# Optimization experiments

Hardware: AMD Instinct MI355X
Metric: run time of the kernel (lower is better)

Reference implementation:

```python
import jax, jax.numpy as jnp
import numpy as np

N_REVIEWS = 500000
N_ITEMS = 100000
N_USERS = 200000
D = 128           # per-entity embedding dim
INPUT_DIM = 3 * D # 384
OUTPUT_DIM = 128


def setup_inputs() -> dict:
    key = jax.random.key(0)
    k1, k2, k3, k4, k5, k6 = jax.random.split(key, 6)
    review_embedding = jax.random.normal(k1, (N_REVIEWS, D), dtype=jnp.float32)
    item_embedding = jax.random.normal(k2, (N_ITEMS, D), dtype=jnp.float32)
    user_embedding = jax.random.normal(k3, (N_USERS, D), dtype=jnp.float32)
    adj_user_idx = jax.random.randint(k4, (N_REVIEWS,), 0, N_USERS, dtype=jnp.int32)
    adj_item_idx = jax.random.randint(k5, (N_REVIEWS,), 0, N_ITEMS, dtype=jnp.int32)
    agg_weights = jax.random.normal(k6, (INPUT_DIM, OUTPUT_DIM), dtype=jnp.float32) * 0.05
    return {
        "review_embedding": review_embedding,
        "item_embedding": item_embedding,
        "user_embedding": user_embedding,
        "adj_user_idx": adj_user_idx,
        "adj_item_idx": adj_item_idx,
        "agg_weights": agg_weights,
    }


def reference(review_embedding, item_embedding, user_embedding,
              adj_user_idx, adj_item_idx, agg_weights):
    # Gather neighbor embeddings (tf.nn.embedding_lookup)
    review_item = item_embedding[adj_item_idx]  # [N_reviews, D]
    review_user = user_embedding[adj_user_idx]  # [N_reviews, D]
    # Concat along feature axis -> [N_reviews, 3D], then dense + activation
    agg_vector = jnp.concatenate([review_embedding, review_user, review_item], axis=1)
    return jax.nn.relu(agg_vector @ agg_weights)
```

## Files before the change

### kernel.cpp

```cpp
#include <hip/hip_runtime.h>
#include <hip/hip_bf16.h>

#define NREV 500000
#define DIM  128
#define KDIM 384

typedef __attribute__((ext_vector_type(4))) float f32x4;
typedef __attribute__((ext_vector_type(8))) short bf16x8;

__device__ __forceinline__ unsigned short f2bf_s(float x) {
    unsigned int u = __builtin_bit_cast(unsigned int, x);
    u = (u + 0x7FFFu + ((u >> 16) & 1u)) >> 16;
    return (unsigned short)u;
}

__global__ void wconv_kernel(const float* __restrict__ W,
                             unsigned short* __restrict__ Bw) {
    int e = blockIdx.x * 256 + threadIdx.x;
    if (e < 12 * 8 * 64 * 8) {
        int j  = e & 7;
        int l  = (e >> 3) & 63;
        int fg = (e >> 9) & 7;
        int ks = e >> 12;
        int n = fg * 16 + (l & 15);
        int k = ks * 32 + ((l >> 4) << 3) + j;
        Bw[e] = f2bf_s(W[k * DIM + n]);
    }
}

__device__ __forceinline__ void gload_lds16(const void* g, void* l) {
    __builtin_amdgcn_global_load_lds(
        (const __attribute__((address_space(1))) void*)g,
        (__attribute__((address_space(3))) void*)l, 16, 0, 0);
}

__device__ __forceinline__ unsigned int pktrunc(float lo, float hi) {
    unsigned int a = __builtin_bit_cast(unsigned int, lo);
    unsigned int b = __builtin_bit_cast(unsigned int, hi);
    return (b & 0xFFFF0000u) | (a >> 16);
}
__device__ __forceinline__ bf16x8 cvt8(f32x4 a, f32x4 b) {
    union { bf16x8 v; unsigned int u[4]; } U;
    U.u[0] = pktrunc(a[0], a[1]);
    U.u[1] = pktrunc(a[2], a[3]);
    U.u[2] = pktrunc(b[0], b[1]);
    U.u[3] = pktrunc(b[2], b[3]);
    return U.v;
}

__global__ __launch_bounds__(256, 2) void agg_kernel(
    const float* __restrict__ rev,
    const float* __restrict__ item,
    const float* __restrict__ user,
    const int*   __restrict__ uidx,
    const int*   __restrict__ iidx,
    const unsigned short* __restrict__ Bw,
    float* __restrict__ out)
{
    __shared__ __align__(16) float          Atile[3][128 * 32];
    __shared__ __align__(16) unsigned short Btile[3][4096];

    const int r0   = blockIdx.x * 128;
    const int t    = threadIdx.x;
    const int wid  = t >> 6, lane = t & 63;
    const int wr   = wid >> 1, wc = wid & 1;
    const int lm   = lane & 15, lk = lane >> 4;

    const int srow = t >> 3;
    const int cswz = ((t & 7) ^ ((t >> 3) & 7)) << 2;

    const float* pr[4]; const float* pu[4]; const float* pi[4];
    #pragma unroll
    for (int it = 0; it < 4; ++it) {
        int gr = r0 + it * 32 + srow;
        if (gr >= NREV) gr = NREV - 1;
        pr[it] = rev  + (size_t)gr * DIM + cswz;
        pu[it] = user + (size_t)uidx[gr] * DIM + cswz;
        pi[it] = item + (size_t)iidx[gr] * DIM + cswz;
    }

    f32x4 acc[4][4];
    #pragma unroll
    for (int i = 0; i < 4; ++i)
        #pragma unroll
        for (int j = 0; j < 4; ++j)
            acc[i][j] = (f32x4){0.f, 0.f, 0.f, 0.f};

    const int axor  = (lm & 7) << 4;
    const int koff0 = (lk * 32) ^ axor;

    auto prefetch = [&](int s, int buf) {
        const int cb = (s & 3) * 32;
        #pragma unroll
        for (int it = 0; it < 4; ++it) {
            const float* src = ((s < 4) ? pr[it] : (s < 8) ? pu[it] : pi[it]) + cb;
            gload_lds16(src, (char*)&Atile[buf][0] + it * 4096 + t * 16);
        }
        #pragma unroll
        for (int it = 0; it < 2; ++it) {
            gload_lds16((const char*)Bw + s * 8192 + it * 4096 + t * 16,
                        (char*)&Btile[buf][0] + it * 4096 + t * 16);
        }
    };

    auto step = [&](int s) {
        const char*           la = (const char*)&Atile[s % 3][0];
        const unsigned short* lb = &Btile[s % 3][0];
        bf16x8 bfrag[4];
        #pragma unroll
        for (int nf = 0; nf < 4; ++nf)
            bfrag[nf] = *reinterpret_cast<const bf16x8*>(
                lb + (((wc * 4 + nf) * 64 + lane) << 3));
        #pragma unroll
        for (int mf = 0; mf < 4; ++mf) {
            int rb = (wr * 64 + mf * 16 + lm) * 128;
            f32x4 f0 = *reinterpret_cast<const f32x4*>(la + rb + koff0);
            f32x4 f1 = *reinterpret_cast<const f32x4*>(la + rb + (koff0 ^ 16));
            bf16x8 af = cvt8(f0, f1);
            #pragma unroll
            for (int nf = 0; nf < 4; ++nf)
                acc[mf][nf] = __builtin_amdgcn_mfma_f32_16x16x32_bf16(
                    af, bfrag[nf], acc[mf][nf], 0, 0, 0);
        }
    };

    prefetch(0, 0);
    prefetch(1, 1);

    #pragma unroll
    for (int s = 0; s < 12; ++s) {
        if (s == 11) { asm volatile("s_waitcnt vmcnt(0)" ::: "memory"); }
        else         { asm volatile("s_waitcnt vmcnt(6)" ::: "memory"); }
        __builtin_amdgcn_s_barrier();
        asm volatile("" ::: "memory");
        if (s < 10) prefetch(s + 2, (s + 2) % 3);
        step(s);
    }

    #pragma unroll
    for (int mf = 0; mf < 4; ++mf) {
        #pragma unroll
        for (int j = 0; j < 4; ++j) {
            int row = r0 + wr * 64 + mf * 16 + lk * 4 + j;
            if (row < NREV) {
                float* orow = out + (size_t)row * DIM + wc * 64;
                #pragma unroll
                for (int nf = 0; nf < 4; ++nf)
                    orow[nf * 16 + lm] = fmaxf(acc[mf][nf][j], 0.0f);
            }
        }
    }
}

extern "C" void kernel_launch(void* const* d_in, const int* in_sizes, int n_in,
                              void* d_out, int out_size, void* d_ws, size_t ws_size,
                              hipStream_t stream) {
    const float* rev  = (const float*)d_in[0];
    const float* item = (const float*)d_in[1];
    const float* user = (const float*)d_in[2];
    const int*   uidx = (const int*)d_in[3];
    const int*   iidx = (const int*)d_in[4];
    const float* W    = (const float*)d_in[5];
    unsigned short* Bw = (unsigned short*)d_ws;
    float* out = (float*)d_out;

    wconv_kernel<<<192, 256, 0, stream>>>(W, Bw);

    int nblocks = (NREV + 127) / 128;
    agg_kernel<<<nblocks, 256, 0, stream>>>(rev, item, user, uidx, iidx, Bw, out);
}
```

Before: 179.1 us.

## Load A and B fragments directly from global memory, dropping the LDS pipeline

Removes the triple-buffered LDS staging with global_load_lds and barriers. Each lane now loads its own A fragment rows and B fragments straight from global memory into registers, relying on the fully unrolled loop for latency hiding. s_setprio is added around the MFMA block, and the fp32-to-bf16 truncation now uses a single perm instruction per pair. This saves LDS traffic and block-wide synchronisation, but each wave reloads the gathered rows and weights that were previously shared, and coalescing becomes worse since each lane fetches 32-byte chunks.

```diff
diff --git a/kernel.cpp b/kernel.cpp
--- a/kernel.cpp
+++ b/kernel.cpp
@@ -28,23 +28,17 @@
     }
 }
 
-__device__ __forceinline__ void gload_lds16(const void* g, void* l) {
-    __builtin_amdgcn_global_load_lds(
-        (const __attribute__((address_space(1))) void*)g,
-        (__attribute__((address_space(3))) void*)l, 16, 0, 0);
-}
-
-__device__ __forceinline__ unsigned int pktrunc(float lo, float hi) {
-    unsigned int a = __builtin_bit_cast(unsigned int, lo);
-    unsigned int b = __builtin_bit_cast(unsigned int, hi);
-    return (b & 0xFFFF0000u) | (a >> 16);
+__device__ __forceinline__ unsigned int pk2(float lo, float hi) {
+    return __builtin_amdgcn_perm(__builtin_bit_cast(unsigned int, hi),
+                                 __builtin_bit_cast(unsigned int, lo),
+                                 0x07060302u);
 }
 __device__ __forceinline__ bf16x8 cvt8(f32x4 a, f32x4 b) {
     union { bf16x8 v; unsigned int u[4]; } U;
-    U.u[0] = pktrunc(a[0], a[1]);
-    U.u[1] = pktrunc(a[2], a[3]);
-    U.u[2] = pktrunc(b[0], b[1]);
-    U.u[3] = pktrunc(b[2], b[3]);
+    U.u[0] = pk2(a[0], a[1]);
+    U.u[1] = pk2(a[2], a[3]);
+    U.u[2] = pk2(b[0], b[1]);
+    U.u[3] = pk2(b[2], b[3]);
     return U.v;
 }
 
@@ -57,26 +51,20 @@
     const unsigned short* __restrict__ Bw,
     float* __restrict__ out)
 {
-    __shared__ __align__(16) float          Atile[3][128 * 32];
-    __shared__ __align__(16) unsigned short Btile[3][4096];
-
-    const int r0   = blockIdx.x * 128;
     const int t    = threadIdx.x;
     const int wid  = t >> 6, lane = t & 63;
     const int wr   = wid >> 1, wc = wid & 1;
     const int lm   = lane & 15, lk = lane >> 4;
+    const int r0   = blockIdx.x * 128;
 
-    const int srow = t >> 3;
-    const int cswz = ((t & 7) ^ ((t >> 3) & 7)) << 2;
-
-    const float* pr[4]; const float* pu[4]; const float* pi[4];
+    const float* baseA[3][4];
     #pragma unroll
-    for (int it = 0; it < 4; ++it) {
-        int gr = r0 + it * 32 + srow;
-        if (gr >= NREV) gr = NREV - 1;
-        pr[it] = rev  + (size_t)gr * DIM + cswz;
-        pu[it] = user + (size_t)uidx[gr] * DIM + cswz;
-        pi[it] = item + (size_t)iidx[gr] * DIM + cswz;
+    for (int mf = 0; mf < 4; ++mf) {
+        int r = r0 + wr * 64 + mf * 16 + lm;
+        if (r >= NREV) r = NREV - 1;
+        baseA[0][mf] = rev  + (size_t)r * DIM + lk * 8;
+        baseA[1][mf] = user + (size_t)uidx[r] * DIM + lk * 8;
+        baseA[2][mf] = item + (size_t)iidx[r] * DIM + lk * 8;
     }
 
     f32x4 acc[4][4];
@@ -86,55 +74,33 @@
         for (int j = 0; j < 4; ++j)
             acc[i][j] = (f32x4){0.f, 0.f, 0.f, 0.f};
 
-    const int axor  = (lm & 7) << 4;
-    const int koff0 = (lk * 32) ^ axor;
+    const unsigned short* bbase = Bw + ((wc * 4) * 64 + lane) * 8;
 
-    auto prefetch = [&](int s, int buf) {
-        const int cb = (s & 3) * 32;
+    #pragma unroll
+    for (int s = 0; s < 12; ++s) {
+        f32x4 a0[4], a1[4];
         #pragma unroll
-        for (int it = 0; it < 4; ++it) {
-            const float* src = ((s < 4) ? pr[it] : (s < 8) ? pu[it] : pi[it]) + cb;
-            gload_lds16(src, (char*)&Atile[buf][0] + it * 4096 + t * 16);
+        for (int mf = 0; mf < 4; ++mf) {
+            const float* p = baseA[s >> 2][mf] + (s & 3) * 32;
+            a0[mf] = *reinterpret_cast<const f32x4*>(p);
+            a1[mf] = *reinterpret_cast<const f32x4*>(p + 4);
         }
-        #pragma unroll
-        for (int it = 0; it < 2; ++it) {
-            gload_lds16((const char*)Bw + s * 8192 + it * 4096 + t * 16,
-                        (char*)&Btile[buf][0] + it * 4096 + t * 16);
-        }
-    };
-
-    auto step = [&](int s) {
-        const char*           la = (const char*)&Atile[s % 3][0];
-        const unsigned short* lb = &Btile[s % 3][0];
         bf16x8 bfrag[4];
         #pragma unroll
         for (int nf = 0; nf < 4; ++nf)
             bfrag[nf] = *reinterpret_cast<const bf16x8*>(
-                lb + (((wc * 4 + nf) * 64 + lane) << 3));
+                bbase + (size_t)(s * 8 + nf) * 64 * 8);
+
+        __builtin_amdgcn_s_setprio(1);
         #pragma unroll
         for (int mf = 0; mf < 4; ++mf) {
-            int rb = (wr * 64 + mf * 16 + lm) * 128;
-            f32x4 f0 = *reinterpret_cast<const f32x4*>(la + rb + koff0);
-            f32x4 f1 = *reinterpret_cast<const f32x4*>(la + rb + (koff0 ^ 16));
-            bf16x8 af = cvt8(f0, f1);
+            bf16x8 af = cvt8(a0[mf], a1[mf]);
             #pragma unroll
             for (int nf = 0; nf < 4; ++nf)
                 acc[mf][nf] = __builtin_amdgcn_mfma_f32_16x16x32_bf16(
                     af, bfrag[nf], acc[mf][nf], 0, 0, 0);
         }
-    };
-
-    prefetch(0, 0);
-    prefetch(1, 1);
-
-    #pragma unroll
-    for (int s = 0; s < 12; ++s) {
-        if (s == 11) { asm volatile("s_waitcnt vmcnt(0)" ::: "memory"); }
-        else         { asm volatile("s_waitcnt vmcnt(6)" ::: "memory"); }
-        __builtin_amdgcn_s_barrier();
-        asm volatile("" ::: "memory");
-        if (s < 10) prefetch(s + 2, (s + 2) % 3);
-        step(s);
+        __builtin_amdgcn_s_setprio(0);
     }
 
     #pragma unroll
```

Result: slower. 266.2 us (+48.6%).

## Load weight fragments directly into registers instead of staging through LDS

Applied to the files above, without the earlier changes.

The bf16 weight fragments now go straight from global memory into per-wave registers, triple-buffered, rather than being copied into shared-memory tiles and read back. This cuts LDS footprint and LDS read traffic, and the occupancy hint is raised from 2 to 3 blocks per CU. The bf16 truncation packing now uses a single byte-permute instruction. The cost is higher VGPR pressure from 12 extra vector registers of B fragments, and per-wave redundant global/L2 reads of the weights.

```diff
diff --git a/kernel.cpp b/kernel.cpp
--- a/kernel.cpp
+++ b/kernel.cpp
@@ -34,21 +34,21 @@
         (__attribute__((address_space(3))) void*)l, 16, 0, 0);
 }
 
-__device__ __forceinline__ unsigned int pktrunc(float lo, float hi) {
-    unsigned int a = __builtin_bit_cast(unsigned int, lo);
-    unsigned int b = __builtin_bit_cast(unsigned int, hi);
-    return (b & 0xFFFF0000u) | (a >> 16);
+__device__ __forceinline__ unsigned int pk2(float lo, float hi) {
+    return __builtin_amdgcn_perm(__builtin_bit_cast(unsigned int, hi),
+                                 __builtin_bit_cast(unsigned int, lo),
+                                 0x07060302u);
 }
 __device__ __forceinline__ bf16x8 cvt8(f32x4 a, f32x4 b) {
     union { bf16x8 v; unsigned int u[4]; } U;
-    U.u[0] = pktrunc(a[0], a[1]);
-    U.u[1] = pktrunc(a[2], a[3]);
-    U.u[2] = pktrunc(b[0], b[1]);
-    U.u[3] = pktrunc(b[2], b[3]);
+    U.u[0] = pk2(a[0], a[1]);
+    U.u[1] = pk2(a[2], a[3]);
+    U.u[2] = pk2(b[0], b[1]);
+    U.u[3] = pk2(b[2], b[3]);
     return U.v;
 }
 
-__global__ __launch_bounds__(256, 2) void agg_kernel(
+__global__ __launch_bounds__(256, 3) void agg_kernel(
     const float* __restrict__ rev,
     const float* __restrict__ item,
     const float* __restrict__ user,
@@ -57,8 +57,7 @@
     const unsigned short* __restrict__ Bw,
     float* __restrict__ out)
 {
-    __shared__ __align__(16) float          Atile[3][128 * 32];
-    __shared__ __align__(16) unsigned short Btile[3][4096];
+    __shared__ __align__(16) float Atile[3][128 * 32];
 
     const int r0   = blockIdx.x * 128;
     const int t    = threadIdx.x;
@@ -88,29 +87,27 @@
 
     const int axor  = (lm & 7) << 4;
     const int koff0 = (lk * 32) ^ axor;
+    const unsigned short* bbase = Bw + ((wc * 4) * 64 + lane) * 8;
 
-    auto prefetch = [&](int s, int buf) {
+    auto prefetchA = [&](int s, int buf) {
         const int cb = (s & 3) * 32;
         #pragma unroll
         for (int it = 0; it < 4; ++it) {
             const float* src = ((s < 4) ? pr[it] : (s < 8) ? pu[it] : pi[it]) + cb;
             gload_lds16(src, (char*)&Atile[buf][0] + it * 4096 + t * 16);
         }
+    };
+    bf16x8 breg[3][4];
+    auto loadB = [&](int s, bf16x8* dst) {
         #pragma unroll
-        for (int it = 0; it < 2; ++it) {
-            gload_lds16((const char*)Bw + s * 8192 + it * 4096 + t * 16,
-                        (char*)&Btile[buf][0] + it * 4096 + t * 16);
-        }
+        for (int nf = 0; nf < 4; ++nf)
+            dst[nf] = *reinterpret_cast<const bf16x8*>(
+                bbase + (size_t)(s * 8 + nf) * 512);
     };
 
     auto step = [&](int s) {
-        const char*           la = (const char*)&Atile[s % 3][0];
-        const unsigned short* lb = &Btile[s % 3][0];
-        bf16x8 bfrag[4];
-        #pragma unroll
-        for (int nf = 0; nf < 4; ++nf)
-            bfrag[nf] = *reinterpret_cast<const bf16x8*>(
-                lb + (((wc * 4 + nf) * 64 + lane) << 3));
+        const char* la = (const char*)&Atile[s % 3][0];
+        const bf16x8* bf = breg[s % 3];
         #pragma unroll
         for (int mf = 0; mf < 4; ++mf) {
             int rb = (wr * 64 + mf * 16 + lm) * 128;
@@ -120,20 +117,23 @@
             #pragma unroll
             for (int nf = 0; nf < 4; ++nf)
                 acc[mf][nf] = __builtin_amdgcn_mfma_f32_16x16x32_bf16(
-                    af, bfrag[nf], acc[mf][nf], 0, 0, 0);
+                    af, bf[nf], acc[mf][nf], 0, 0, 0);
         }
     };
 
-    prefetch(0, 0);
-    prefetch(1, 1);
+    prefetchA(0, 0); loadB(0, breg[0]);
+    prefetchA(1, 1); loadB(1, breg[1]);
 
     #pragma unroll
     for (int s = 0; s < 12; ++s) {
         if (s == 11) { asm volatile("s_waitcnt vmcnt(0)" ::: "memory"); }
-        else         { asm volatile("s_waitcnt vmcnt(6)" ::: "memory"); }
+        else         { asm volatile("s_waitcnt vmcnt(8)" ::: "memory"); }
         __builtin_amdgcn_s_barrier();
         asm volatile("" ::: "memory");
-        if (s < 10) prefetch(s + 2, (s + 2) % 3);
+        if (s < 10) {
+            prefetchA(s + 2, (s + 2) % 3);
+            loadB(s + 2, breg[(s + 2) % 3]);
+        }
         step(s);
     }
 
```

Measured after the change: 182.4 us. No clear change (+1.8%).
